# Kernel optimization log

Hardware: AMD Instinct MI355X
Metric: run time of the kernel (lower is better)

Reference implementation:

```python
import jax, jax.numpy as jnp
import numpy as np

HIDDEN = 2048
HEADS = 16
HEAD_DIM = HIDDEN // HEADS          # 128
HALF = HEAD_DIM // 2                # 64
LATENT = HIDDEN // 4                # 512 (compression_ratio=4)
ROPE_BASE = 10000.0


def _rope_cos_sin(seq_len):
    # LlamaRotaryEmbedding with dim=HALF
    inv_freq = 1.0 / (ROPE_BASE ** (jnp.arange(0, HALF, 2, dtype=jnp.float32) / HALF))
    t = jnp.arange(seq_len, dtype=jnp.float32)
    freqs = jnp.einsum('i,j->ij', t, inv_freq)          # [S, HALF/2]
    emb = jnp.concatenate([freqs, freqs], axis=-1)       # [S, HALF]
    cos = jnp.cos(emb)[None, :, None, :]                 # [1,S,1,HALF]
    sin = jnp.sin(emb)[None, :, None, :]
    return cos, sin


def _rotate_half(x):
    x1, x2 = jnp.split(x, 2, axis=-1)
    return jnp.concatenate([-x2, x1], axis=-1)


def _apply_rope(x, cos, sin):
    return x * cos + _rotate_half(x) * sin


def setup_inputs() -> dict:
    key = jax.random.key(0)
    ks = jax.random.split(key, 10)
    B, S = 2, 2048
    std = 0.02
    inp = {
        'x':        jax.random.normal(ks[0], (B, S, HIDDEN), jnp.float32),
        # weights stored as [in, out] (transposed torch Linear weight)
        'W_kv_d':   jax.random.normal(ks[1], (HIDDEN, LATENT), jnp.float32) * std,
        'W_q_d':    jax.random.normal(ks[2], (HIDDEN, LATENT), jnp.float32) * std,
        'W_k_u':    jax.random.normal(ks[3], (LATENT, HEADS * HALF), jnp.float32) * std,
        'W_q_u':    jax.random.normal(ks[4], (LATENT, HEADS * HALF), jnp.float32) * std,
        'W_v_u':    jax.random.normal(ks[5], (LATENT, HIDDEN), jnp.float32) * std,
        'W_rope_k': jax.random.normal(ks[6], (HIDDEN, HIDDEN // 2), jnp.float32) * std,
        'W_rope_q': jax.random.normal(ks[7], (LATENT, HIDDEN // 2), jnp.float32) * std,
        'W_o':      jax.random.normal(ks[8], (HIDDEN, HIDDEN), jnp.float32) * std,
    }
    return inp


def reference(x, W_kv_d, W_q_d, W_k_u, W_q_u, W_v_u, W_rope_k, W_rope_q, W_o):
    B, S, _ = x.shape
    kv_latent = x @ W_kv_d                      # [B,S,LATENT]
    q_latent = x @ W_q_d                        # [B,S,LATENT]

    k = (kv_latent @ W_k_u).reshape(B, S, HEADS, HALF)
    q = (q_latent @ W_q_u).reshape(B, S, HEADS, HALF)
    v = (kv_latent @ W_v_u).reshape(B, S, HEADS, HEAD_DIM)

    q_rope = (q_latent @ W_rope_q).reshape(B, S, HEADS, HALF)
    k_rope = (x @ W_rope_k).reshape(B, S, HEADS, HALF)

    cos, sin = _rope_cos_sin(S)
    k_rope = _apply_rope(k_rope, cos, sin)
    q_rope = _apply_rope(q_rope, cos, sin)

    q = jnp.concatenate([q, q_rope], axis=-1)   # [B,S,H,HEAD_DIM]
    k = jnp.concatenate([k, k_rope], axis=-1)

    scale = 1.0 / jnp.sqrt(jnp.float32(HEAD_DIM))
    scores = jnp.einsum('bqhd,bkhd->bhqk', q, k) * scale   # [B,H,S,S]
    causal = jnp.tril(jnp.ones((S, S), dtype=bool))
    scores = jnp.where(causal[None, None], scores, jnp.float32(-1e30))
    attn = jax.nn.softmax(scores, axis=-1)
    y = jnp.einsum('bhqk,bkhd->bqhd', attn, v).reshape(B, S, HIDDEN)
    return y @ W_o
```

## Files before the change

kernel.cpp:

```cpp
#include <hip/hip_runtime.h>
#include <hip/hip_bf16.h>

typedef __hip_bfloat16 bf16;
typedef __attribute__((ext_vector_type(8))) short short8;
typedef __attribute__((ext_vector_type(4))) float f32x4;

#define AS1 __attribute__((address_space(1)))
#define AS3 __attribute__((address_space(3)))

__device__ __forceinline__ void gload_lds16(const bf16* gp, bf16* lp) {
  __builtin_amdgcn_global_load_lds((const AS1 void*)gp, (AS3 void*)lp, 16, 0, 0);
}

__device__ __forceinline__ float fast_exp2(float x) {
#if __has_builtin(__builtin_amdgcn_exp2f)
  return __builtin_amdgcn_exp2f(x);
#else
  return exp2f(x);
#endif
}

__device__ __forceinline__ void store_c(bf16* C, size_t idx, float v) { C[idx] = __float2bfloat16(v); }
__device__ __forceinline__ void store_c(float* C, size_t idx, float v) { C[idx] = v; }

struct __align__(8) b16x4 { bf16 a, b, c, d; };

__global__ void cvt_f32_bf16(const float* __restrict__ in, bf16* __restrict__ out) {
  const int i = (blockIdx.x * 256 + threadIdx.x) * 4;
  const float4 v = *(const float4*)(in + i);
  out[i + 0] = __float2bfloat16(v.x);
  out[i + 1] = __float2bfloat16(v.y);
  out[i + 2] = __float2bfloat16(v.z);
  out[i + 3] = __float2bfloat16(v.w);
}

struct PrepArgs {
  const float* src[8];
  bf16* dst[8];
  int R[8], C[8], cum[8];
};

__global__ void prep_kernel(PrepArgs a) {
  __shared__ bf16 t[32][33];
  const int blk = blockIdx.x;
  int e = 0;
  while (e < 7 && blk >= a.cum[e]) ++e;
  const int lt = blk - (e ? a.cum[e - 1] : 0);
  const int R = a.R[e], C = a.C[e];
  const int tpr = C >> 5;
  const int bx = lt % tpr, by = lt / tpr;
  const float* in = a.src[e];
  bf16* out = a.dst[e];
  const int c0 = bx * 32, r0 = by * 32;
  const int tx = threadIdx.x, ty = threadIdx.y;
  for (int i = 0; i < 4; ++i)
    t[ty + 8 * i][tx] = __float2bfloat16(in[(size_t)(r0 + ty + 8 * i) * C + c0 + tx]);
  __syncthreads();
  for (int i = 0; i < 4; ++i)
    out[(size_t)(c0 + ty + 8 * i) * R + r0 + tx] = t[tx][ty + 8 * i];
}

template <typename CT, int MODE>
__global__ void gemm_bt(const bf16* __restrict__ A, int lda,
                        const bf16* __restrict__ Bt,
                        CT* __restrict__ C, bf16* __restrict__ C2, int ldc,
                        int K)
{
  __shared__ __align__(16) bf16 As[128 * 32];
  __shared__ __align__(16) bf16 Bs[128 * 32];
  const int tid  = threadIdx.x;
  const int wave = tid >> 6, lane = tid & 63;
  const int quad = lane >> 4, l16 = lane & 15;
  const int m0 = blockIdx.y * 128, n0 = blockIdx.x * 128;
  const int wm = (wave >> 1) * 64, wn = (wave & 1) * 64;

  f32x4 acc[4][4];
#pragma unroll
  for (int i = 0; i < 4; ++i)
#pragma unroll
    for (int j = 0; j < 4; ++j) acc[i][j] = (f32x4){0.f, 0.f, 0.f, 0.f};

  const int r1  = tid >> 2;
  const int ks1 = (tid & 3) * 8;

  for (int k0 = 0; k0 < K; k0 += 32) {
    gload_lds16(A  + (size_t)(m0 + r1)      * lda + k0 + ks1, &As[tid * 8]);
    gload_lds16(A  + (size_t)(m0 + r1 + 64) * lda + k0 + ks1, &As[(tid + 256) * 8]);
    gload_lds16(Bt + (size_t)(n0 + r1)      * K   + k0 + ks1, &Bs[tid * 8]);
    gload_lds16(Bt + (size_t)(n0 + r1 + 64) * K   + k0 + ks1, &Bs[(tid + 256) * 8]);
    __syncthreads();

    short8 af[4], bf_[4];
#pragma unroll
    for (int mt = 0; mt < 4; ++mt)
      af[mt] = *(const short8*)&As[(wm + mt * 16 + l16) * 32 + quad * 8];
#pragma unroll
    for (int nt = 0; nt < 4; ++nt)
      bf_[nt] = *(const short8*)&Bs[(wn + nt * 16 + l16) * 32 + quad * 8];
#pragma unroll
    for (int mt = 0; mt < 4; ++mt)
#pragma unroll
      for (int nt = 0; nt < 4; ++nt)
        acc[mt][nt] = __builtin_amdgcn_mfma_f32_16x16x32_bf16(af[mt], bf_[nt], acc[mt][nt], 0, 0, 0);
    __syncthreads();
  }

#pragma unroll
  for (int mt = 0; mt < 4; ++mt) {
    const int row = m0 + wm + mt * 16 + quad * 4;
#pragma unroll
    for (int nt = 0; nt < 4; ++nt) {
      const int cn = n0 + wn + nt * 16 + l16;
      const f32x4 v = acc[mt][nt];
      if (MODE == 0) {
#pragma unroll
        for (int r = 0; r < 4; ++r)
          store_c(C, (size_t)(row + r) * ldc + cn, v[r]);
      } else if (MODE == 4) {
        if (cn < 1024) {
#pragma unroll
          for (int r = 0; r < 4; ++r)
            store_c(C, (size_t)(row + r) * 1024 + cn, v[r]);
        } else {
          const int cn2 = cn - 1024;
          const int g = ((cn2 >> 6) << 7) + 64 + (cn2 & 63);
#pragma unroll
          for (int r = 0; r < 4; ++r)
            C2[(size_t)(row + r) * 2048 + g] = __float2bfloat16(v[r]);
        }
      }
    }
  }
}

__global__ void gemm_up_fused(const bf16* __restrict__ latcat,
                              const bf16* __restrict__ wtUP,
                              const bf16* __restrict__ wtQcat,
                              bf16* __restrict__ vT, bf16* __restrict__ kfull,
                              bf16* __restrict__ qfull)
{
  const bool is2 = (blockIdx.x >= 24);
  const bf16* A  = latcat + (is2 ? 512 : 0);
  const bf16* Bt = is2 ? wtQcat : wtUP;
  const int n0 = (is2 ? (int)blockIdx.x - 24 : (int)blockIdx.x) * 128;
  const int K = 512, lda = 1024;

  __shared__ __align__(16) bf16 As[128 * 32];
  __shared__ __align__(16) bf16 Bs[128 * 32];
  const int tid  = threadIdx.x;
  const int wave = tid >> 6, lane = tid & 63;
  const int quad = lane >> 4, l16 = lane & 15;
  const int m0 = blockIdx.y * 128;
  const int wm = (wave >> 1) * 64, wn = (wave & 1) * 64;

  f32x4 acc[4][4];
#pragma unroll
  for (int i = 0; i < 4; ++i)
#pragma unroll
    for (int j = 0; j < 4; ++j) acc[i][j] = (f32x4){0.f, 0.f, 0.f, 0.f};

  const int r1  = tid >> 2;
  const int ks1 = (tid & 3) * 8;

  for (int k0 = 0; k0 < K; k0 += 32) {
    gload_lds16(A  + (size_t)(m0 + r1)      * lda + k0 + ks1, &As[tid * 8]);
    gload_lds16(A  + (size_t)(m0 + r1 + 64) * lda + k0 + ks1, &As[(tid + 256) * 8]);
    gload_lds16(Bt + (size_t)(n0 + r1)      * K   + k0 + ks1, &Bs[tid * 8]);
    gload_lds16(Bt + (size_t)(n0 + r1 + 64) * K   + k0 + ks1, &Bs[(tid + 256) * 8]);
    __syncthreads();

    short8 af[4], bf_[4];
#pragma unroll
    for (int mt = 0; mt < 4; ++mt)
      af[mt] = *(const short8*)&As[(wm + mt * 16 + l16) * 32 + quad * 8];
#pragma unroll
    for (int nt = 0; nt < 4; ++nt)
      bf_[nt] = *(const short8*)&Bs[(wn + nt * 16 + l16) * 32 + quad * 8];
#pragma unroll
    for (int mt = 0; mt < 4; ++mt)
#pragma unroll
      for (int nt = 0; nt < 4; ++nt)
        acc[mt][nt] = __builtin_amdgcn_mfma_f32_16x16x32_bf16(af[mt], bf_[nt], acc[mt][nt], 0, 0, 0);
    __syncthreads();
  }

  if (is2) {
#pragma unroll
    for (int mt = 0; mt < 4; ++mt) {
      const int row = m0 + wm + mt * 16 + quad * 4;
#pragma unroll
      for (int nt = 0; nt < 4; ++nt) {
        const int cn = n0 + wn + nt * 16 + l16;
        const int g = (((cn >> 6) & 15) << 7) + ((cn >> 10) << 6) + (cn & 63);
        const f32x4 v = acc[mt][nt];
#pragma unroll
        for (int r = 0; r < 4; ++r)
          qfull[(size_t)(row + r) * 2048 + g] = __float2bfloat16(v[r]);
      }
    }
  } else {
#pragma unroll
    for (int mt = 0; mt < 4; ++mt) {
      const int row = m0 + wm + mt * 16 + quad * 4;
#pragma unroll
      for (int nt = 0; nt < 4; ++nt) {
        const int cn = n0 + wn + nt * 16 + l16;
        const f32x4 v = acc[mt][nt];
        if (cn < 1024) {
          const int g = ((cn >> 6) << 7) + (cn & 63);
#pragma unroll
          for (int r = 0; r < 4; ++r)
            kfull[(size_t)(row + r) * 2048 + g] = __float2bfloat16(v[r]);
        } else {
          const int cn2 = cn - 1024;
          const int bb = row >> 11, s0 = row & 2047;
          b16x4 pk;
          pk.a = __float2bfloat16(v[0]); pk.b = __float2bfloat16(v[1]);
          pk.c = __float2bfloat16(v[2]); pk.d = __float2bfloat16(v[3]);
          *(b16x4*)(vT + ((size_t)(bb * 2048 + cn2)) * 2048 + s0) = pk;
        }
      }
    }
  }
}

__global__ void rope_kernel(bf16* __restrict__ q, bf16* __restrict__ k)
{
  const int idx = blockIdx.x * 256 + threadIdx.x;
  const int i = idx & 31;
  const int h = (idx >> 5) & 15;
  const int s = (idx >> 9) & 2047;
  const int b = idx >> 20;
  const size_t off = ((size_t)(b * 2048 + s)) * 2048 + h * 128 + 64;
  const float inv = fast_exp2(-(float)i * 0.41524101186092029f);
  const float ang = (float)s * inv;
  const float cs = cosf(ang), sn = sinf(ang);
  {
    bf16* p = q + off;
    const float x1 = __bfloat162float(p[i]);
    const float x2 = __bfloat162float(p[i + 32]);
    p[i]      = __float2bfloat16(x1 * cs - x2 * sn);
    p[i + 32] = __float2bfloat16(x2 * cs + x1 * sn);
  }
  {
    bf16* p = k + off;
    const float x1 = __bfloat162float(p[i]);
    const float x2 = __bfloat162float(p[i + 32]);
    p[i]      = __float2bfloat16(x1 * cs - x2 * sn);
    p[i + 32] = __float2bfloat16(x2 * cs + x1 * sn);
  }
}

__global__ __launch_bounds__(256, 3) void attn6_kernel(
    const bf16* __restrict__ Q, const bf16* __restrict__ Kf,
    const bf16* __restrict__ VT, bf16* __restrict__ Y)
{
  __shared__ __align__(16) bf16 Ks[64][136];
  __shared__ __align__(16) bf16 VTs[128][72];
  __shared__ __align__(16) bf16 Ps[4][16][72];
  const int tid  = threadIdx.x;
  const int wave = tid >> 6, lane = tid & 63;
  const int quad = lane >> 4, l16 = lane & 15;
  const int bh = blockIdx.x;
  const int qt = 31 - blockIdx.y;
  const size_t kqbase = ((size_t)(bh >> 4) * 2048) * 2048 + (bh & 15) * 128;
  const size_t vtbase = (size_t)bh * 128 * 2048;
  const float C2 = 0.08838834764831845f * 1.4426950408889634f;
  const float MNEG = -30.0f;

  short8 ones;
#pragma unroll
  for (int i = 0; i < 8; ++i) ones[i] = (short)0x3F80;

  const int krow = tid >> 4, kcol = (tid & 15) * 8;
  const int vrow = tid >> 3, vcol = (tid & 7) * 8;

  const int q0 = qt * 64;
  const int T = qt + 1;
  const int row0q = q0 + wave * 16 + quad * 4;

  short8 qf[4];
  {
    const bf16* qp = Q + kqbase + (size_t)(q0 + wave * 16 + l16) * 2048 + quad * 8;
#pragma unroll
    for (int kc = 0; kc < 4; ++kc) qf[kc] = *(const short8*)(qp + kc * 32);
  }
  f32x4 o[8];
#pragma unroll
  for (int i = 0; i < 8; ++i) o[i] = (f32x4){0, 0, 0, 0};
  f32x4 lacc = (f32x4){0, 0, 0, 0};

  short8 kg[4], vg[4];
#pragma unroll
  for (int i = 0; i < 4; ++i)
    kg[i] = *(const short8*)(Kf + kqbase + (size_t)(krow + i * 16) * 2048 + kcol);
#pragma unroll
  for (int i = 0; i < 4; ++i)
    vg[i] = *(const short8*)(VT + vtbase + (size_t)(vrow + i * 32) * 2048 + vcol);

  for (int t = 0; t < T; ++t) {
    const int k0 = t * 64;
    __syncthreads();
#pragma unroll
    for (int i = 0; i < 4; ++i) *(short8*)&Ks[krow + i * 16][kcol] = kg[i];
#pragma unroll
    for (int i = 0; i < 4; ++i) *(short8*)&VTs[vrow + i * 32][vcol] = vg[i];
    __syncthreads();
    if (t + 1 < T) {
      const int kn = k0 + 64;
#pragma unroll
      for (int i = 0; i < 4; ++i)
        kg[i] = *(const short8*)(Kf + kqbase + (size_t)(kn + krow + i * 16) * 2048 + kcol);
#pragma unroll
      for (int i = 0; i < 4; ++i)
        vg[i] = *(const short8*)(VT + vtbase + (size_t)(vrow + i * 32) * 2048 + kn + vcol);
    }

    f32x4 sf[4];
#pragma unroll
    for (int kt = 0; kt < 4; ++kt) {
      f32x4 a = (f32x4){0, 0, 0, 0};
#pragma unroll
      for (int kc = 0; kc < 4; ++kc) {
        const short8 bfr = *(const short8*)&Ks[kt * 16 + l16][kc * 32 + quad * 8];
        a = __builtin_amdgcn_mfma_f32_16x16x32_bf16(qf[kc], bfr, a, 0, 0, 0);
      }
      sf[kt] = a;
    }
    if (t == T - 1) {
#pragma unroll
      for (int kt = 0; kt < 4; ++kt) {
        const int col = k0 + kt * 16 + l16;
#pragma unroll
        for (int r = 0; r < 4; ++r)
          sf[kt][r] = (col > row0q + r) ? -3e38f : sf[kt][r];
      }
    }
#pragma unroll
    for (int kt = 0; kt < 4; ++kt)
#pragma unroll
      for (int r = 0; r < 4; ++r) {
        const float p = fast_exp2(__builtin_fmaf(sf[kt][r], C2, MNEG));
        Ps[wave][quad * 4 + r][kt * 16 + l16] = __float2bfloat16(p);
      }
    asm volatile("s_waitcnt lgkmcnt(0)" ::: "memory");
#pragma unroll
    for (int kc = 0; kc < 2; ++kc) {
      const short8 ap = *(const short8*)&Ps[wave][l16][kc * 32 + quad * 8];
      lacc = __builtin_amdgcn_mfma_f32_16x16x32_bf16(ap, ones, lacc, 0, 0, 0);
#pragma unroll
      for (int dt = 0; dt < 8; ++dt) {
        const short8 vb = *(const short8*)&VTs[dt * 16 + l16][kc * 32 + quad * 8];
        o[dt] = __builtin_amdgcn_mfma_f32_16x16x32_bf16(ap, vb, o[dt], 0, 0, 0);
      }
    }
  }

#pragma unroll
  for (int r = 0; r < 4; ++r) {
    const float inv = 1.0f / lacc[r];
#pragma unroll
    for (int dt = 0; dt < 8; ++dt)
      Y[kqbase + (size_t)(row0q + r) * 2048 + dt * 16 + l16] = __float2bfloat16(o[dt][r] * inv);
  }
}

extern "C" void kernel_launch(void* const* d_in, const int* in_sizes, int n_in,
                              void* d_out, int out_size, void* d_ws, size_t ws_size,
                              hipStream_t stream)
{
  const float* x      = (const float*)d_in[0];
  const float* Wkvd   = (const float*)d_in[1];
  const float* Wqd    = (const float*)d_in[2];
  const float* Wku    = (const float*)d_in[3];
  const float* Wqu    = (const float*)d_in[4];
  const float* Wvu    = (const float*)d_in[5];
  const float* Wropek = (const float*)d_in[6];
  const float* Wropeq = (const float*)d_in[7];
  const float* Wo     = (const float*)d_in[8];

  char* ws = (char*)d_ws;
  size_t off = 0;
  auto alloc = [&](size_t elems) {
    bf16* p = (bf16*)(ws + off);
    off += ((elems * sizeof(bf16) + 255) & ~(size_t)255);
    return p;
  };
  bf16* wtX    = alloc((size_t)2048 * 2048);
  bf16* wtUP   = alloc((size_t)3072 * 512);
  bf16* wtQcat = alloc((size_t)2048 * 512);
  bf16* latcat = alloc((size_t)4096 * 1024);
  bf16* wt_o   = alloc((size_t)2048 * 2048);
  bf16* xbf    = alloc((size_t)4096 * 2048);
  bf16* qfull  = alloc((size_t)4096 * 2048);
  bf16* kfull  = alloc((size_t)4096 * 2048);
  bf16* ybuf   = (bf16*)ws;
  bf16* vT     = (bf16*)d_out;
  (void)ws_size; (void)in_sizes; (void)n_in; (void)out_size;

  cvt_f32_bf16<<<8192, 256, 0, stream>>>(x, xbf);

  PrepArgs pa;
  const float* srcs[8] = {Wkvd, Wqd, Wropek, Wku, Wvu, Wqu, Wropeq, Wo};
  bf16* dsts[8] = {wtX, wtX + (size_t)512 * 2048, wtX + (size_t)1024 * 2048,
                   wtUP, wtUP + (size_t)1024 * 512,
                   wtQcat, wtQcat + (size_t)1024 * 512, wt_o};
  const int Rs[8] = {2048, 2048, 2048, 512, 512, 512, 512, 2048};
  const int Cs[8] = {512, 512, 1024, 1024, 2048, 1024, 1024, 2048};
  int cum = 0;
  for (int e = 0; e < 8; ++e) {
    pa.src[e] = srcs[e]; pa.dst[e] = dsts[e]; pa.R[e] = Rs[e]; pa.C[e] = Cs[e];
    cum += (Rs[e] >> 5) * (Cs[e] >> 5);
    pa.cum[e] = cum;
  }
  prep_kernel<<<cum, dim3(32, 8), 0, stream>>>(pa);

  gemm_bt<bf16, 4><<<dim3(16, 32), 256, 0, stream>>>(xbf, 2048, wtX, latcat, kfull, 1024, 2048);
  gemm_up_fused<<<dim3(40, 32), 256, 0, stream>>>(latcat, wtUP, wtQcat, vT, kfull, qfull);

  rope_kernel<<<(2 * 2048 * 16 * 32) / 256, 256, 0, stream>>>(qfull, kfull);
  attn6_kernel<<<dim3(32, 32), 256, 0, stream>>>(qfull, kfull, vT, ybuf);
  gemm_bt<float, 0><<<dim3(16, 32), 256, 0, stream>>>(ybuf, 2048, wt_o, (float*)d_out, (bf16*)nullptr, 2048, 2048);
}
```

Baseline: 329.8 us.

## Enlarge attention query tile to 128 rows with XOR-swizzled LDS and balanced scheduling

The attention kernel now gives each block 128 query rows, with each wave handling two 16-row M tiles. This doubles reuse of every K/V tile loaded into LDS and halves the number of blocks. LDS padding is replaced by XOR swizzles on the K, V^T and P buffers to avoid bank conflicts, and waves skip K tiles that lie fully above the causal diagonal. Query tiles are reordered so short and long causal blocks are interleaved for load balance. The cost is higher register use (launch bounds drop to 2 blocks per SIMD) and fewer blocks in the grid.

```diff
diff --git a/kernel.cpp b/kernel.cpp
--- a/kernel.cpp
+++ b/kernel.cpp
@@ -251,18 +251,20 @@
   }
 }
 
-__global__ __launch_bounds__(256, 3) void attn6_kernel(
+__global__ __launch_bounds__(256, 2) void attn7_kernel(
     const bf16* __restrict__ Q, const bf16* __restrict__ Kf,
     const bf16* __restrict__ VT, bf16* __restrict__ Y)
 {
-  __shared__ __align__(16) bf16 Ks[64][136];
-  __shared__ __align__(16) bf16 VTs[128][72];
-  __shared__ __align__(16) bf16 Ps[4][16][72];
+  __shared__ __align__(16) bf16 Ks[64 * 128];
+  __shared__ __align__(16) bf16 VTs[128 * 64];
+  __shared__ __align__(16) bf16 Ps[4 * 32 * 64];
   const int tid  = threadIdx.x;
   const int wave = tid >> 6, lane = tid & 63;
   const int quad = lane >> 4, l16 = lane & 15;
   const int bh = blockIdx.x;
-  const int qt = 31 - blockIdx.y;
+  const int yy = blockIdx.y;
+  const int aa = yy & 7;
+  const int qt = (yy >> 3) ? (15 - aa) : aa;
   const size_t kqbase = ((size_t)(bh >> 4) * 2048) * 2048 + (bh & 15) * 128;
   const size_t vtbase = (size_t)bh * 128 * 2048;
   const float C2 = 0.08838834764831845f * 1.4426950408889634f;
@@ -275,20 +277,26 @@
   const int krow = tid >> 4, kcol = (tid & 15) * 8;
   const int vrow = tid >> 3, vcol = (tid & 7) * 8;
 
-  const int q0 = qt * 64;
-  const int T = qt + 1;
-  const int row0q = q0 + wave * 16 + quad * 4;
-
-  short8 qf[4];
-  {
-    const bf16* qp = Q + kqbase + (size_t)(q0 + wave * 16 + l16) * 2048 + quad * 8;
-#pragma unroll
-    for (int kc = 0; kc < 4; ++kc) qf[kc] = *(const short8*)(qp + kc * 32);
-  }
-  f32x4 o[8];
-#pragma unroll
-  for (int i = 0; i < 8; ++i) o[i] = (f32x4){0, 0, 0, 0};
-  f32x4 lacc = (f32x4){0, 0, 0, 0};
+  const int q0 = qt * 128;
+  const int T = 2 * qt + 2;
+  const int wq0 = q0 + wave * 32;
+  const int psbase = wave * (32 * 64);
+
+  short8 qf[2][4];
+#pragma unroll
+  for (int m = 0; m < 2; ++m) {
+    const bf16* qp = Q + kqbase + (size_t)(wq0 + m * 16 + l16) * 2048 + quad * 8;
+#pragma unroll
+    for (int kc = 0; kc < 4; ++kc) qf[m][kc] = *(const short8*)(qp + kc * 32);
+  }
+  f32x4 o[2][8];
+#pragma unroll
+  for (int m = 0; m < 2; ++m)
+#pragma unroll
+    for (int i = 0; i < 8; ++i) o[m][i] = (f32x4){0, 0, 0, 0};
+  f32x4 lacc[2];
+  lacc[0] = (f32x4){0, 0, 0, 0};
+  lacc[1] = (f32x4){0, 0, 0, 0};
 
   short8 kg[4], vg[4];
 #pragma unroll
@@ -302,9 +310,15 @@
     const int k0 = t * 64;
     __syncthreads();
 #pragma unroll
-    for (int i = 0; i < 4; ++i) *(short8*)&Ks[krow + i * 16][kcol] = kg[i];
-#pragma unroll
-    for (int i = 0; i < 4; ++i) *(short8*)&VTs[vrow + i * 32][vcol] = vg[i];
+    for (int i = 0; i < 4; ++i) {
+      const int rw = krow + i * 16;
+      *(short8*)&Ks[rw * 128 + (kcol ^ ((rw & 7) * 8))] = kg[i];
+    }
+#pragma unroll
+    for (int i = 0; i < 4; ++i) {
+      const int rw = vrow + i * 32;
+      *(short8*)&VTs[rw * 64 + (vcol ^ ((rw & 7) * 8))] = vg[i];
+    }
     __syncthreads();
     if (t + 1 < T) {
       const int kn = k0 + 64;
@@ -316,52 +330,78 @@
         vg[i] = *(const short8*)(VT + vtbase + (size_t)(vrow + i * 32) * 2048 + kn + vcol);
     }
 
-    f32x4 sf[4];
-#pragma unroll
-    for (int kt = 0; kt < 4; ++kt) {
-      f32x4 a = (f32x4){0, 0, 0, 0};
-#pragma unroll
-      for (int kc = 0; kc < 4; ++kc) {
-        const short8 bfr = *(const short8*)&Ks[kt * 16 + l16][kc * 32 + quad * 8];
-        a = __builtin_amdgcn_mfma_f32_16x16x32_bf16(qf[kc], bfr, a, 0, 0, 0);
-      }
-      sf[kt] = a;
-    }
-    if (t == T - 1) {
+    if (k0 <= wq0 + 31) {
+      f32x4 sf[2][4];
+#pragma unroll
+      for (int m = 0; m < 2; ++m)
+#pragma unroll
+        for (int kt = 0; kt < 4; ++kt) sf[m][kt] = (f32x4){0, 0, 0, 0};
 #pragma unroll
       for (int kt = 0; kt < 4; ++kt) {
-        const int col = k0 + kt * 16 + l16;
-#pragma unroll
-        for (int r = 0; r < 4; ++r)
-          sf[kt][r] = (col > row0q + r) ? -3e38f : sf[kt][r];
-      }
-    }
-#pragma unroll
-    for (int kt = 0; kt < 4; ++kt)
-#pragma unroll
-      for (int r = 0; r < 4; ++r) {
-        const float p = fast_exp2(__builtin_fmaf(sf[kt][r], C2, MNEG));
-        Ps[wave][quad * 4 + r][kt * 16 + l16] = __float2bfloat16(p);
-      }
-    asm volatile("s_waitcnt lgkmcnt(0)" ::: "memory");
-#pragma unroll
-    for (int kc = 0; kc < 2; ++kc) {
-      const short8 ap = *(const short8*)&Ps[wave][l16][kc * 32 + quad * 8];
-      lacc = __builtin_amdgcn_mfma_f32_16x16x32_bf16(ap, ones, lacc, 0, 0, 0);
-#pragma unroll
-      for (int dt = 0; dt < 8; ++dt) {
-        const short8 vb = *(const short8*)&VTs[dt * 16 + l16][kc * 32 + quad * 8];
-        o[dt] = __builtin_amdgcn_mfma_f32_16x16x32_bf16(ap, vb, o[dt], 0, 0, 0);
-      }
-    }
-  }
-
-#pragma unroll
-  for (int r = 0; r < 4; ++r) {
-    const float inv = 1.0f / lacc[r];
-#pragma unroll
-    for (int dt = 0; dt < 8; ++dt)
-      Y[kqbase + (size_t)(row0q + r) * 2048 + dt * 16 + l16] = __float2bfloat16(o[dt][r] * inv);
+#pragma unroll
+        for (int kc = 0; kc < 4; ++kc) {
+          const short8 bfr = *(const short8*)&Ks[(kt * 16 + l16) * 128 +
+                                                ((kc * 32 + quad * 8) ^ ((l16 & 7) * 8))];
+          sf[0][kt] = __builtin_amdgcn_mfma_f32_16x16x32_bf16(qf[0][kc], bfr, sf[0][kt], 0, 0, 0);
+          sf[1][kt] = __builtin_amdgcn_mfma_f32_16x16x32_bf16(qf[1][kc], bfr, sf[1][kt], 0, 0, 0);
+        }
+      }
+#pragma unroll
+      for (int m = 0; m < 2; ++m) {
+        const int row0m = wq0 + m * 16 + quad * 4;
+        if (k0 + 63 > row0m) {
+#pragma unroll
+          for (int kt = 0; kt < 4; ++kt) {
+            const int col = k0 + kt * 16 + l16;
+#pragma unroll
+            for (int r = 0; r < 4; ++r)
+              sf[m][kt][r] = (col > row0m + r) ? -3e38f : sf[m][kt][r];
+          }
+        }
+      }
+#pragma unroll
+      for (int m = 0; m < 2; ++m)
+#pragma unroll
+        for (int kt = 0; kt < 4; ++kt)
+#pragma unroll
+          for (int r = 0; r < 4; ++r) {
+            const float p = fast_exp2(__builtin_fmaf(sf[m][kt][r], C2, MNEG));
+            const int prow = m * 16 + quad * 4 + r;
+            const int pcol = (kt * 16 + l16) ^ (quad * 16);
+            Ps[psbase + prow * 64 + pcol] = __float2bfloat16(p);
+          }
+      asm volatile("s_waitcnt lgkmcnt(0)" ::: "memory");
+#pragma unroll
+      for (int kc = 0; kc < 2; ++kc) {
+        short8 ap[2];
+#pragma unroll
+        for (int m = 0; m < 2; ++m) {
+          const int acol = (kc * 32 + quad * 8) ^ (((l16 >> 2) & 3) * 16);
+          ap[m] = *(const short8*)&Ps[psbase + (m * 16 + l16) * 64 + acol];
+          lacc[m] = __builtin_amdgcn_mfma_f32_16x16x32_bf16(ap[m], ones, lacc[m], 0, 0, 0);
+        }
+#pragma unroll
+        for (int dt = 0; dt < 8; ++dt) {
+          const short8 vb = *(const short8*)&VTs[(dt * 16 + l16) * 64 +
+                                                ((kc * 32 + quad * 8) ^ ((l16 & 7) * 8))];
+          o[0][dt] = __builtin_amdgcn_mfma_f32_16x16x32_bf16(ap[0], vb, o[0][dt], 0, 0, 0);
+          o[1][dt] = __builtin_amdgcn_mfma_f32_16x16x32_bf16(ap[1], vb, o[1][dt], 0, 0, 0);
+        }
+      }
+    }
+  }
+
+#pragma unroll
+  for (int m = 0; m < 2; ++m) {
+    const int row0m = wq0 + m * 16 + quad * 4;
+#pragma unroll
+    for (int r = 0; r < 4; ++r) {
+      const float inv = 1.0f / lacc[m][r];
+#pragma unroll
+      for (int dt = 0; dt < 8; ++dt)
+        Y[kqbase + (size_t)(row0m + r) * 2048 + dt * 16 + l16] =
+            __float2bfloat16(o[m][dt][r] * inv);
+    }
   }
 }
 
@@ -419,6 +459,6 @@
   gemm_up_fused<<<dim3(40, 32), 256, 0, stream>>>(latcat, wtUP, wtQcat, vT, kfull, qfull);
 
   rope_kernel<<<(2 * 2048 * 16 * 32) / 256, 256, 0, stream>>>(qfull, kfull);
-  attn6_kernel<<<dim3(32, 32), 256, 0, stream>>>(qfull, kfull, vT, ybuf);
+  attn7_kernel<<<dim3(32, 16), 256, 0, stream>>>(qfull, kfull, vT, ybuf);
   gemm_bt<float, 0><<<dim3(16, 32), 256, 0, stream>>>(ybuf, 2048, wt_o, (float*)d_out, (bf16*)nullptr, 2048, 2048);
 }
```

Result: no change. 331.2 us (+0.4%).
